# Kernel optimization log

Measured on AMD Instinct MI355X. Metric: run time of the kernel, lower is better.

Reference implementation:

```python
import jax, jax.numpy as jnp
import numpy as np

ALPHA = 0.2  # LeakyReLU negative slope


def setup_inputs() -> dict:
    key = jax.random.key(0)
    k1, k2, k3, k4 = jax.random.split(key, 4)
    N, Fin, Fout = 8192, 256, 64
    inputs = {
        "input": jax.random.normal(k1, (N, Fin), dtype=jnp.float32),
        "adj": jax.random.randint(k2, (N, N), 0, 2, dtype=jnp.int32),
        "W": jax.random.normal(k3, (Fin, Fout), dtype=jnp.float32) * (1.414 * np.sqrt(2.0 / (Fin + Fout))),
        "a": jax.random.normal(k4, (2 * Fout, 1), dtype=jnp.float32) * (1.414 * np.sqrt(2.0 / (2 * Fout + 1))),
    }
    return inputs


def reference(input, adj, W, a):
    # h: [N, Fout]
    h = input @ W
    Fout = h.shape[1]
    # Decompose pairwise score: e[i,j] = leakyrelu(h[i]@a1 + h[j]@a2)
    # (mathematically identical to the original concat+matmul construction,
    #  but avoids the O(N^2 * 2F) intermediate)
    a1, a2 = a[:Fout, 0], a[Fout:, 0]
    s1 = h @ a1  # [N]
    s2 = h @ a2  # [N]
    e = jax.nn.leaky_relu(s1[:, None] + s2[None, :], negative_slope=ALPHA)  # [N, N]
    # Mask non-edges with -10 (as in the original), row softmax
    masked = jnp.where(adj > 0, e, jnp.float32(-10.0))
    attention = jax.nn.softmax(masked, axis=1)
    # dropout p=0.0 (eval/reference mode): identity
    h_prime = attention @ h  # [N, Fout]
    return jax.nn.elu(h_prime)  # concat=True path
```

## Files before the change

### kernel.cpp

```cpp
#include <hip/hip_runtime.h>
#include <hip/hip_bf16.h>
#include <cstdint>
#include <cstddef>

#define NN 8192
#define FIN 256
#define FOUT 64
#define ALPHA_SLOPE 0.2f

#define JT 128
#define LDW 136
#define JSPLIT 8
#define IT 64
#define CP 68

typedef short s16x8 __attribute__((ext_vector_type(8)));
typedef float f32x4 __attribute__((ext_vector_type(4)));

__device__ __forceinline__ unsigned short f2bf(float x) {
    union { float f; uint32_t u; } v; v.f = x;
    uint32_t u = v.u;
    return (unsigned short)((u + 0x7FFFu + ((u >> 16) & 1u)) >> 16);
}

__global__ __launch_bounds__(256) void k_h(
    const float* __restrict__ input, const float* __restrict__ W,
    const float* __restrict__ a,
    unsigned short* __restrict__ htg, float* __restrict__ s1, float* __restrict__ s2)
{
    const int wid  = threadIdx.x >> 6;
    const int lane = threadIdx.x & 63;
    const int i    = blockIdx.x * 4 + wid;
    const float* inrow = input + (size_t)i * FIN;

    float acc = 0.f;
    #pragma unroll 8
    for (int c = 0; c < FIN; c += 4) {
        float4 x = *(const float4*)(inrow + c);
        acc = fmaf(x.x, W[(c + 0) * FOUT + lane], acc);
        acc = fmaf(x.y, W[(c + 1) * FOUT + lane], acc);
        acc = fmaf(x.z, W[(c + 2) * FOUT + lane], acc);
        acc = fmaf(x.w, W[(c + 3) * FOUT + lane], acc);
    }
    htg[(size_t)lane * NN + i] = f2bf(acc);

    float v1 = acc * a[lane];
    float v2 = acc * a[FOUT + lane];
    #pragma unroll
    for (int off = 32; off; off >>= 1) {
        v1 += __shfl_xor(v1, off);
        v2 += __shfl_xor(v2, off);
    }
    if (lane == 0) { s1[i] = v1; s2[i] = v2; }
}

__global__ __launch_bounds__(256) void k_attn(
    const int* __restrict__ adj,
    const unsigned short* __restrict__ htg,
    const float* __restrict__ s1g, const float* __restrict__ s2g,
    float* __restrict__ slabs)
{
    __shared__ __align__(16) unsigned short Wt[IT * LDW];
    __shared__ __align__(16) unsigned short Ht[80 * LDW];

    const int t  = threadIdx.x;
    const int bi = blockIdx.x >> 3;
    const int js = blockIdx.x & 7;
    const int i0 = bi * IT;
    const int jbase = js * (NN / JSPLIT);

    {
        int n = 64 + (t >> 4);
        int c = (t & 15) * 8;
        unsigned short val = (n == 64) ? (unsigned short)0x3F80 : (unsigned short)0;
        unsigned int p = (unsigned int)val | ((unsigned int)val << 16);
        uint4 q; q.x = q.y = q.z = q.w = p;
        *(uint4*)&Ht[n * LDW + c] = q;
    }

    const int wid  = t >> 6;
    const int lane = t & 63;
    const int m    = lane & 15;
    const int quad = lane >> 4;

    f32x4 acc0 = {0,0,0,0}, acc1 = {0,0,0,0}, acc2 = {0,0,0,0},
          acc3 = {0,0,0,0}, acc4 = {0,0,0,0};

    const int wr0 = t >> 6;
    const int wc  = (t & 63) * 2;

    for (int tile = 0; tile < (NN / JSPLIT) / JT; ++tile) {
        const int j0 = jbase + tile * JT;
        __syncthreads();

        {
            int c = (t & 15) * 8;
            #pragma unroll
            for (int p = 0; p < 4; ++p) {
                int n = (t >> 4) + p * 16;
                uint4 q = *(const uint4*)(htg + (size_t)n * NN + j0 + c);
                *(uint4*)&Ht[n * LDW + c] = q;
            }
        }
        {
            float2 s2p = *(const float2*)(s2g + j0 + wc);
            #pragma unroll
            for (int rr = 0; rr < 16; ++rr) {
                int r = wr0 + rr * 4;
                float s1v = s1g[i0 + r];
                int2 av = *(const int2*)(adj + (size_t)(i0 + r) * NN + j0 + wc);
                float x0 = s1v + s2p.x;
                float x1 = s1v + s2p.y;
                float e0 = (av.x > 0) ? fmaxf(x0, ALPHA_SLOPE * x0) : -10.0f;
                float e1 = (av.y > 0) ? fmaxf(x1, ALPHA_SLOPE * x1) : -10.0f;
                unsigned int pk = (unsigned int)f2bf(__expf(e0))
                                | ((unsigned int)f2bf(__expf(e1)) << 16);
                *(unsigned int*)&Wt[r * LDW + wc] = pk;
            }
        }
        __syncthreads();

        const unsigned short* wbase = Wt + (wid * 16 + m) * LDW + quad * 8;
        const unsigned short* hbase = Ht + m * LDW + quad * 8;
        #pragma unroll
        for (int ko = 0; ko < JT; ko += 32) {
            s16x8 af = *(const s16x8*)(wbase + ko);
            s16x8 b0 = *(const s16x8*)(hbase + ko);
            s16x8 b1 = *(const s16x8*)(hbase + 16 * LDW + ko);
            s16x8 b2 = *(const s16x8*)(hbase + 32 * LDW + ko);
            s16x8 b3 = *(const s16x8*)(hbase + 48 * LDW + ko);
            s16x8 b4 = *(const s16x8*)(hbase + 64 * LDW + ko);
            acc0 = __builtin_amdgcn_mfma_f32_16x16x32_bf16(af, b0, acc0, 0, 0, 0);
            acc1 = __builtin_amdgcn_mfma_f32_16x16x32_bf16(af, b1, acc1, 0, 0, 0);
            acc2 = __builtin_amdgcn_mfma_f32_16x16x32_bf16(af, b2, acc2, 0, 0, 0);
            acc3 = __builtin_amdgcn_mfma_f32_16x16x32_bf16(af, b3, acc3, 0, 0, 0);
            acc4 = __builtin_amdgcn_mfma_f32_16x16x32_bf16(af, b4, acc4, 0, 0, 0);
        }
    }

    float* slab = slabs + (size_t)js * ((size_t)NN * CP);
    const int irow0 = i0 + wid * 16 + quad * 4;
    #pragma unroll
    for (int reg = 0; reg < 4; ++reg) {
        size_t irow = (size_t)(irow0 + reg) * CP;
        slab[irow +  0 + m] = acc0[reg];
        slab[irow + 16 + m] = acc1[reg];
        slab[irow + 32 + m] = acc2[reg];
        slab[irow + 48 + m] = acc3[reg];
        if (m == 0) slab[irow + 64] = acc4[reg];
    }
}

__global__ __launch_bounds__(256) void k_norm(
    const float* __restrict__ slabs, float* __restrict__ out)
{
    int gid = blockIdx.x * 256 + threadIdx.x;
    int i = gid >> 6, k = gid & 63;
    float num = 0.f, den = 0.f;
    #pragma unroll
    for (int js = 0; js < JSPLIT; ++js) {
        const float* row = slabs + (size_t)js * ((size_t)NN * CP) + (size_t)i * CP;
        num += row[k];
        den += row[64];
    }
    float v = num / den;
    out[gid] = (v > 0.f) ? v : (__expf(v) - 1.f);
}

extern "C" void kernel_launch(void* const* d_in, const int* in_sizes, int n_in,
                              void* d_out, int out_size, void* d_ws, size_t ws_size,
                              hipStream_t stream) {
    const float* input = (const float*)d_in[0];
    const int*   adj   = (const int*)d_in[1];
    const float* W     = (const float*)d_in[2];
    const float* a     = (const float*)d_in[3];
    float* out = (float*)d_out;

    char* ws = (char*)d_ws;
    float* slabs = (float*)ws;
    size_t off = (size_t)JSPLIT * NN * CP * sizeof(float);
    unsigned short* htg = (unsigned short*)(ws + off);
    off += (size_t)FOUT * NN * sizeof(unsigned short);
    float* s1 = (float*)(ws + off); off += NN * sizeof(float);
    float* s2 = (float*)(ws + off);

    k_h   <<<NN / 4, 256, 0, stream>>>(input, W, a, htg, s1, s2);
    k_attn<<<(NN / IT) * JSPLIT, 256, 0, stream>>>(adj, htg, s1, s2, slabs);
    k_norm<<<NN * FOUT / 256, 256, 0, stream>>>(slabs, out);
}
```

Before: 459.0 us.

## Drop LDS staging in attention kernel; build MFMA operands directly in registers

```diff
diff --git a/kernel.cpp b/kernel.cpp
--- a/kernel.cpp
+++ b/kernel.cpp
@@ -7,11 +7,9 @@
 #define FIN 256
 #define FOUT 64
 #define ALPHA_SLOPE 0.2f
+#define EXP_M10 4.5399929762484854e-05f
 
-#define JT 128
-#define LDW 136
 #define JSPLIT 8
-#define IT 64
 #define CP 68
 
 typedef short s16x8 __attribute__((ext_vector_type(8)));
@@ -28,30 +26,50 @@
     const float* __restrict__ a,
     unsigned short* __restrict__ htg, float* __restrict__ s1, float* __restrict__ s2)
 {
+    __shared__ __align__(16) unsigned short tile[64][28];
     const int wid  = threadIdx.x >> 6;
     const int lane = threadIdx.x & 63;
-    const int i    = blockIdx.x * 4 + wid;
-    const float* inrow = input + (size_t)i * FIN;
+    const int i0   = blockIdx.x * 16;
+    const int r0   = wid * 4;
+    const float* inb = input + (size_t)(i0 + r0) * FIN;
 
-    float acc = 0.f;
-    #pragma unroll 8
+    float acc0 = 0.f, acc1 = 0.f, acc2 = 0.f, acc3 = 0.f;
+    #pragma unroll 4
     for (int c = 0; c < FIN; c += 4) {
-        float4 x = *(const float4*)(inrow + c);
-        acc = fmaf(x.x, W[(c + 0) * FOUT + lane], acc);
-        acc = fmaf(x.y, W[(c + 1) * FOUT + lane], acc);
-        acc = fmaf(x.z, W[(c + 2) * FOUT + lane], acc);
-        acc = fmaf(x.w, W[(c + 3) * FOUT + lane], acc);
+        float w0 = W[(c + 0) * FOUT + lane];
+        float w1 = W[(c + 1) * FOUT + lane];
+        float w2 = W[(c + 2) * FOUT + lane];
+        float w3 = W[(c + 3) * FOUT + lane];
+        float4 x0 = *(const float4*)(inb + 0 * FIN + c);
+        float4 x1 = *(const float4*)(inb + 1 * FIN + c);
+        float4 x2 = *(const float4*)(inb + 2 * FIN + c);
+        float4 x3 = *(const float4*)(inb + 3 * FIN + c);
+        acc0 = fmaf(x0.x, w0, fmaf(x0.y, w1, fmaf(x0.z, w2, fmaf(x0.w, w3, acc0))));
+        acc1 = fmaf(x1.x, w0, fmaf(x1.y, w1, fmaf(x1.z, w2, fmaf(x1.w, w3, acc1))));
+        acc2 = fmaf(x2.x, w0, fmaf(x2.y, w1, fmaf(x2.z, w2, fmaf(x2.w, w3, acc2))));
+        acc3 = fmaf(x3.x, w0, fmaf(x3.y, w1, fmaf(x3.z, w2, fmaf(x3.w, w3, acc3))));
     }
-    htg[(size_t)lane * NN + i] = f2bf(acc);
 
-    float v1 = acc * a[lane];
-    float v2 = acc * a[FOUT + lane];
+    const float a1v = a[lane], a2v = a[FOUT + lane];
+    float accs[4] = {acc0, acc1, acc2, acc3};
     #pragma unroll
-    for (int off = 32; off; off >>= 1) {
-        v1 += __shfl_xor(v1, off);
-        v2 += __shfl_xor(v2, off);
+    for (int r = 0; r < 4; ++r) {
+        float v1 = accs[r] * a1v;
+        float v2 = accs[r] * a2v;
+        #pragma unroll
+        for (int off = 32; off; off >>= 1) {
+            v1 += __shfl_xor(v1, off);
+            v2 += __shfl_xor(v2, off);
+        }
+        if (lane == 0) { s1[i0 + r0 + r] = v1; s2[i0 + r0 + r] = v2; }
+        tile[lane][r0 + r] = f2bf(accs[r]);
     }
-    if (lane == 0) { s1[i] = v1; s2[i] = v2; }
+    __syncthreads();
+
+    const int feat = threadIdx.x >> 2;
+    const int cg   = (threadIdx.x & 3) * 4;
+    uint2 q = *(const uint2*)&tile[feat][cg];
+    *(uint2*)(htg + (size_t)feat * NN + i0 + cg) = q;
 }
 
 __global__ __launch_bounds__(256) void k_attn(
@@ -60,94 +78,79 @@
     const float* __restrict__ s1g, const float* __restrict__ s2g,
     float* __restrict__ slabs)
 {
-    __shared__ __align__(16) unsigned short Wt[IT * LDW];
-    __shared__ __align__(16) unsigned short Ht[80 * LDW];
-
-    const int t  = threadIdx.x;
-    const int bi = blockIdx.x >> 3;
-    const int js = blockIdx.x & 7;
-    const int i0 = bi * IT;
-    const int jbase = js * (NN / JSPLIT);
-
-    {
-        int n = 64 + (t >> 4);
-        int c = (t & 15) * 8;
-        unsigned short val = (n == 64) ? (unsigned short)0x3F80 : (unsigned short)0;
-        unsigned int p = (unsigned int)val | ((unsigned int)val << 16);
-        uint4 q; q.x = q.y = q.z = q.w = p;
-        *(uint4*)&Ht[n * LDW + c] = q;
-    }
-
+    const int t    = threadIdx.x;
     const int wid  = t >> 6;
     const int lane = t & 63;
+    const int gw   = blockIdx.x * 4 + wid;
+    const int mi   = gw >> 3;
+    const int js   = gw & 7;
     const int m    = lane & 15;
     const int quad = lane >> 4;
+    const int irow = mi * 16 + m;
+    const int jb   = js * (NN / JSPLIT) + quad * 8;
+
+    const float s1v = s1g[irow];
+
+    const short bd = (m == 0) ? (short)0x3F80 : (short)0;
+    const s16x8 bden = {bd, bd, bd, bd, bd, bd, bd, bd};
 
     f32x4 acc0 = {0,0,0,0}, acc1 = {0,0,0,0}, acc2 = {0,0,0,0},
           acc3 = {0,0,0,0}, acc4 = {0,0,0,0};
 
-    const int wr0 = t >> 6;
-    const int wc  = (t & 63) * 2;
+    const int*   aptr = adj + (size_t)irow * NN + jb;
+    const float* s2p  = s2g + jb;
+    const unsigned short* h0 = htg + (size_t)(m +  0) * NN + jb;
+    const unsigned short* h1 = htg + (size_t)(m + 16) * NN + jb;
+    const unsigned short* h2 = htg + (size_t)(m + 32) * NN + jb;
+    const unsigned short* h3 = htg + (size_t)(m + 48) * NN + jb;
 
-    for (int tile = 0; tile < (NN / JSPLIT) / JT; ++tile) {
-        const int j0 = jbase + tile * JT;
-        __syncthreads();
+    #pragma unroll 2
+    for (int ko = 0; ko < (NN / JSPLIT) / 32; ++ko) {
+        int4   av0 = *(const int4*)(aptr);
+        int4   av1 = *(const int4*)(aptr + 4);
+        float4 sa  = *(const float4*)(s2p);
+        float4 sb  = *(const float4*)(s2p + 4);
+        s16x8  b0  = *(const s16x8*)(h0);
+        s16x8  b1  = *(const s16x8*)(h1);
+        s16x8  b2  = *(const s16x8*)(h2);
+        s16x8  b3  = *(const s16x8*)(h3);
 
-        {
-            int c = (t & 15) * 8;
-            #pragma unroll
-            for (int p = 0; p < 4; ++p) {
-                int n = (t >> 4) + p * 16;
-                uint4 q = *(const uint4*)(htg + (size_t)n * NN + j0 + c);
-                *(uint4*)&Ht[n * LDW + c] = q;
-            }
-        }
-        {
-            float2 s2p = *(const float2*)(s2g + j0 + wc);
-            #pragma unroll
-            for (int rr = 0; rr < 16; ++rr) {
-                int r = wr0 + rr * 4;
-                float s1v = s1g[i0 + r];
-                int2 av = *(const int2*)(adj + (size_t)(i0 + r) * NN + j0 + wc);
-                float x0 = s1v + s2p.x;
-                float x1 = s1v + s2p.y;
-                float e0 = (av.x > 0) ? fmaxf(x0, ALPHA_SLOPE * x0) : -10.0f;
-                float e1 = (av.y > 0) ? fmaxf(x1, ALPHA_SLOPE * x1) : -10.0f;
-                unsigned int pk = (unsigned int)f2bf(__expf(e0))
-                                | ((unsigned int)f2bf(__expf(e1)) << 16);
-                *(unsigned int*)&Wt[r * LDW + wc] = pk;
-            }
-        }
-        __syncthreads();
+        float x0 = s1v + sa.x, x1 = s1v + sa.y, x2 = s1v + sa.z, x3 = s1v + sa.w;
+        float x4 = s1v + sb.x, x5 = s1v + sb.y, x6 = s1v + sb.z, x7 = s1v + sb.w;
+        float w0 = (av0.x > 0) ? __expf(fmaxf(x0, ALPHA_SLOPE * x0)) : EXP_M10;
+        float w1 = (av0.y > 0) ? __expf(fmaxf(x1, ALPHA_SLOPE * x1)) : EXP_M10;
+        float w2 = (av0.z > 0) ? __expf(fmaxf(x2, ALPHA_SLOPE * x2)) : EXP_M10;
+        float w3 = (av0.w > 0) ? __expf(fmaxf(x3, ALPHA_SLOPE * x3)) : EXP_M10;
+        float w4 = (av1.x > 0) ? __expf(fmaxf(x4, ALPHA_SLOPE * x4)) : EXP_M10;
+        float w5 = (av1.y > 0) ? __expf(fmaxf(x5, ALPHA_SLOPE * x5)) : EXP_M10;
+        float w6 = (av1.z > 0) ? __expf(fmaxf(x6, ALPHA_SLOPE * x6)) : EXP_M10;
+        float w7 = (av1.w > 0) ? __expf(fmaxf(x7, ALPHA_SLOPE * x7)) : EXP_M10;
 
-        const unsigned short* wbase = Wt + (wid * 16 + m) * LDW + quad * 8;
-        const unsigned short* hbase = Ht + m * LDW + quad * 8;
-        #pragma unroll
-        for (int ko = 0; ko < JT; ko += 32) {
-            s16x8 af = *(const s16x8*)(wbase + ko);
-            s16x8 b0 = *(const s16x8*)(hbase + ko);
-            s16x8 b1 = *(const s16x8*)(hbase + 16 * LDW + ko);
-            s16x8 b2 = *(const s16x8*)(hbase + 32 * LDW + ko);
-            s16x8 b3 = *(const s16x8*)(hbase + 48 * LDW + ko);
-            s16x8 b4 = *(const s16x8*)(hbase + 64 * LDW + ko);
-            acc0 = __builtin_amdgcn_mfma_f32_16x16x32_bf16(af, b0, acc0, 0, 0, 0);
-            acc1 = __builtin_amdgcn_mfma_f32_16x16x32_bf16(af, b1, acc1, 0, 0, 0);
-            acc2 = __builtin_amdgcn_mfma_f32_16x16x32_bf16(af, b2, acc2, 0, 0, 0);
-            acc3 = __builtin_amdgcn_mfma_f32_16x16x32_bf16(af, b3, acc3, 0, 0, 0);
-            acc4 = __builtin_amdgcn_mfma_f32_16x16x32_bf16(af, b4, acc4, 0, 0, 0);
-        }
+        s16x8 af;
+        af[0] = (short)f2bf(w0); af[1] = (short)f2bf(w1);
+        af[2] = (short)f2bf(w2); af[3] = (short)f2bf(w3);
+        af[4] = (short)f2bf(w4); af[5] = (short)f2bf(w5);
+        af[6] = (short)f2bf(w6); af[7] = (short)f2bf(w7);
+
+        acc0 = __builtin_amdgcn_mfma_f32_16x16x32_bf16(af, b0,   acc0, 0, 0, 0);
+        acc1 = __builtin_amdgcn_mfma_f32_16x16x32_bf16(af, b1,   acc1, 0, 0, 0);
+        acc2 = __builtin_amdgcn_mfma_f32_16x16x32_bf16(af, b2,   acc2, 0, 0, 0);
+        acc3 = __builtin_amdgcn_mfma_f32_16x16x32_bf16(af, b3,   acc3, 0, 0, 0);
+        acc4 = __builtin_amdgcn_mfma_f32_16x16x32_bf16(af, bden, acc4, 0, 0, 0);
+
+        aptr += 32; s2p += 32; h0 += 32; h1 += 32; h2 += 32; h3 += 32;
     }
 
     float* slab = slabs + (size_t)js * ((size_t)NN * CP);
-    const int irow0 = i0 + wid * 16 + quad * 4;
+    const int r0 = mi * 16 + quad * 4;
     #pragma unroll
     for (int reg = 0; reg < 4; ++reg) {
-        size_t irow = (size_t)(irow0 + reg) * CP;
-        slab[irow +  0 + m] = acc0[reg];
-        slab[irow + 16 + m] = acc1[reg];
-        slab[irow + 32 + m] = acc2[reg];
-        slab[irow + 48 + m] = acc3[reg];
-        if (m == 0) slab[irow + 64] = acc4[reg];
+        size_t ro = (size_t)(r0 + reg) * CP;
+        slab[ro +  0 + m] = acc0[reg];
+        slab[ro + 16 + m] = acc1[reg];
+        slab[ro + 32 + m] = acc2[reg];
+        slab[ro + 48 + m] = acc3[reg];
+        if (m == 0) slab[ro + 64] = acc4[reg];
     }
 }
 
@@ -184,7 +187,7 @@
     float* s1 = (float*)(ws + off); off += NN * sizeof(float);
     float* s2 = (float*)(ws + off);
 
-    k_h   <<<NN / 4, 256, 0, stream>>>(input, W, a, htg, s1, s2);
-    k_attn<<<(NN / IT) * JSPLIT, 256, 0, stream>>>(adj, htg, s1, s2, slabs);
+    k_h   <<<NN / 16, 256, 0, stream>>>(input, W, a, htg, s1, s2);
+    k_attn<<<(NN / 16) * JSPLIT / 4, 256, 0, stream>>>(adj, htg, s1, s2, slabs);
     k_norm<<<NN * FOUT / 256, 256, 0, stream>>>(slabs, out);
 }
```

Result: no change. 455.1 us (-0.9%).
